# Kernel tuning notes

Hardware: AMD Instinct MI355X
Metric: run time of the kernel (lower is better)

Reference implementation:

```python
import jax, jax.numpy as jnp
import numpy as np
from jax import lax

STRIDES = (8, 16, 32, 64, 128)
LEVEL_HW = ((100, 128), (50, 64), (25, 32), (13, 16), (7, 8))
NUM_CLASSES = 80
PRE_NMS_THRESH = 0.05
PRE_NMS_TOPK = 1000
NMS_THRESH = 0.6
MAX_DET = 100
CLS_OFFSET = 1.0e4  # > max image coordinate, separates classes for joint NMS


def setup_inputs() -> dict:
    key = jax.random.key(0)
    B = 16
    ks = jax.random.split(key, 3 * len(LEVEL_HW))
    inp = {}
    i = 0
    for lvl, (h, w) in enumerate(LEVEL_HW):
        # shift logits down so sigmoid scores are mostly below the 0.05 candidate
        # threshold (realistic detection sparsity)
        inp[f"logits_p{lvl + 3}"] = jax.random.normal(ks[i], (B, NUM_CLASSES, h, w), jnp.float32) - 4.0; i += 1
        inp[f"bbox_p{lvl + 3}"] = jax.random.uniform(ks[i], (B, 4, h, w), jnp.float32, minval=0.0, maxval=64.0); i += 1
        inp[f"ctr_p{lvl + 3}"] = jax.random.normal(ks[i], (B, 1, h, w), jnp.float32); i += 1
    inp["im_info"] = jnp.tile(jnp.array([[800.0, 1024.0]], jnp.float32), (B, 1))
    return inp


def _locations(h, w, stride):
    # FCOSLocation: center of each stride cell -> [HW, 2] as (x, y)
    sx = jnp.arange(w, dtype=jnp.float32) * stride + stride // 2
    sy = jnp.arange(h, dtype=jnp.float32) * stride + stride // 2
    yy, xx = jnp.meshgrid(sy, sx, indexing="ij")
    return jnp.stack([xx.reshape(-1), yy.reshape(-1)], axis=-1)


def _nms_single(boxes, scores, classes):
    # boxes [K,4], scores [K] (descending), classes [K] int
    off = classes.astype(jnp.float32)[:, None] * CLS_OFFSET
    nb = boxes + off  # class-offset trick -> per-class NMS in one pass
    areas = jnp.maximum(nb[:, 2] - nb[:, 0], 0.0) * jnp.maximum(nb[:, 3] - nb[:, 1], 0.0)

    def body(sc, _):
        i = jnp.argmax(sc)
        s = sc[i]
        bi = nb[i]
        xx1 = jnp.maximum(bi[0], nb[:, 0])
        yy1 = jnp.maximum(bi[1], nb[:, 1])
        xx2 = jnp.minimum(bi[2], nb[:, 2])
        yy2 = jnp.minimum(bi[3], nb[:, 3])
        inter = jnp.maximum(xx2 - xx1, 0.0) * jnp.maximum(yy2 - yy1, 0.0)
        iou = inter / (areas[i] + areas - inter + 1e-9)
        sc2 = jnp.where(iou >= NMS_THRESH, -jnp.inf, sc).at[i].set(-jnp.inf)
        return sc2, (i, s > 0.0)

    _, (idxs, valid) = lax.scan(body, scores, None, length=MAX_DET)
    det = jnp.concatenate(
        [boxes[idxs], scores[idxs][:, None], classes[idxs].astype(jnp.float32)[:, None]],
        axis=-1,
    )  # [MAX_DET, 6] = x1,y1,x2,y2,score,class
    return jnp.where(valid[:, None], det, 0.0)


def _forward(logits_p3, bbox_p3, ctr_p3, logits_p4, bbox_p4, ctr_p4,
             logits_p5, bbox_p5, ctr_p5, logits_p6, bbox_p6, ctr_p6,
             logits_p7, bbox_p7, ctr_p7, im_info):
    levels = [(logits_p3, bbox_p3, ctr_p3), (logits_p4, bbox_p4, ctr_p4),
              (logits_p5, bbox_p5, ctr_p5), (logits_p6, bbox_p6, ctr_p6),
              (logits_p7, bbox_p7, ctr_p7)]
    scores_l, boxes_l = [], []
    for (lg, rg, ct), stride in zip(levels, STRIDES):
        B, C, H, W = lg.shape
        cls = jax.nn.sigmoid(lg).transpose(0, 2, 3, 1).reshape(B, H * W, C)
        cen = jax.nn.sigmoid(ct).transpose(0, 2, 3, 1).reshape(B, H * W, 1)
        # candidate threshold on raw class prob, then modulate by centerness
        comb = jnp.where(cls > PRE_NMS_THRESH, cls * cen, 0.0)
        locs = _locations(H, W, stride)  # [HW, 2]
        reg = rg.transpose(0, 2, 3, 1).reshape(B, H * W, 4)  # (l, t, r, b)
        bx = jnp.stack([locs[None, :, 0] - reg[..., 0],
                        locs[None, :, 1] - reg[..., 1],
                        locs[None, :, 0] + reg[..., 2],
                        locs[None, :, 1] + reg[..., 3]], axis=-1)
        scores_l.append(comb)
        boxes_l.append(bx)
    scores = jnp.concatenate(scores_l, axis=1)  # [B, N, C]
    boxes = jnp.concatenate(boxes_l, axis=1)    # [B, N, 4]
    B, N, C = scores.shape
    vals, idx = lax.top_k(scores.reshape(B, N * C), PRE_NMS_TOPK)  # [B, K]
    loc = idx // C
    cls_id = idx % C
    cand = jnp.take_along_axis(boxes, loc[..., None], axis=1)  # [B, K, 4]
    h = im_info[:, 0:1]
    w = im_info[:, 1:2]
    x1 = jnp.clip(cand[..., 0], 0.0, w - 1.0)
    y1 = jnp.clip(cand[..., 1], 0.0, h - 1.0)
    x2 = jnp.clip(cand[..., 2], 0.0, w - 1.0)
    y2 = jnp.clip(cand[..., 3], 0.0, h - 1.0)
    cand = jnp.stack([x1, y1, x2, y2], axis=-1)
    sc = jnp.where(vals > 0.0, jnp.sqrt(jnp.maximum(vals, 0.0) + 1e-12), 0.0)
    return jax.vmap(_nms_single)(cand, sc, cls_id)  # [B, MAX_DET, 6]


def reference(logits_p3, bbox_p3, ctr_p3, logits_p4, bbox_p4, ctr_p4,
              logits_p5, bbox_p5, ctr_p5, logits_p6, bbox_p6, ctr_p6,
              logits_p7, bbox_p7, ctr_p7, im_info):
    return _forward(logits_p3, bbox_p3, ctr_p3, logits_p4, bbox_p4, ctr_p4,
                    logits_p5, bbox_p5, ctr_p5, logits_p6, bbox_p6, ctr_p6,
                    logits_p7, bbox_p7, ctr_p7, im_info)
```

## Files before the change

### kernel.cpp

```cpp
#include <hip/hip_runtime.h>
#include <math.h>

#pragma clang fp contract(off)

#define NB 16
#define NC 80
#define NTOT 17064
#define TOPK 1000
#define NBINS 8192
#define CAP 4096
#define MAXDET 100
#define CNTSTRIDE 64
#define CHUNK 128
#define GH 128
#define SEGCAP 768
#define FB 16

struct Ptrs {
    const float* lg[5];
    const float* bb[5];
    const float* ct[5];
};

__device__ __forceinline__ void level_of(int n, int& l, int& hw, int& W,
                                         int& stride, int& half, int& HW) {
    if (n < 12800)      { l = 0; hw = n;         W = 128; stride = 8;   half = 4;  HW = 12800; }
    else if (n < 16000) { l = 1; hw = n - 12800; W = 64;  stride = 16;  half = 8;  HW = 3200;  }
    else if (n < 16800) { l = 2; hw = n - 16000; W = 32;  stride = 32;  half = 16; HW = 800;   }
    else if (n < 17008) { l = 3; hw = n - 16800; W = 16;  stride = 64;  half = 32; HW = 208;   }
    else                { l = 4; hw = n - 17008; W = 8;   stride = 128; half = 64; HW = 56;    }
}

__device__ __forceinline__ float fast_sig(float x) {
    float e = __expf(-x);
    return __builtin_amdgcn_rcpf(1.0f + e);
}

#define HG_ELEM(X, CT, J, CC, NB0)                                            \
    if ((X) > -2.47f) {                             \
        float cls = fast_sig(X);                                              \
        float cen = fast_sig(CT);                                             \
        unsigned bits = __float_as_uint(cls * cen);                           \
        if (bits >= FB_LO) {                                                  \
            int lb = (int)((bits - 32u) >> 19) - BINBASE;                     \
            lb = (lb < 0) ? 0 : ((lb > 63) ? 63 : lb);                        \
            atomicAdd(&whv[lb], 1u);                                          \
            unsigned pos = atomicAdd(s_na, 1u);                               \
            if (pos < SEGCAP) {                                               \
                unsigned idx = (unsigned)(((NB0) + (J)) * NC + (CC));         \
                segb[pos] = ((unsigned long long)bits << 32) | idx;           \
            }                                                                 \
        }                                                                     \
    }

template<int HW4, int NF4, int LVOFF>
__device__ __forceinline__ void histg_level(const float* lgb, const float* ctb,
        int tid, int bx, int gx, unsigned FB_LO, int BINBASE, unsigned* whv,
        unsigned* s_na, unsigned long long* segb) {
    for (int i0 = bx * 512; i0 < NF4; i0 += gx * 512) {
        int ia = i0 + tid, ib = i0 + 256 + tid;
        bool la = ia < NF4, lb2 = ib < NF4;
        float4 va = make_float4(-9.f, -9.f, -9.f, -9.f);
        float4 vb = make_float4(-9.f, -9.f, -9.f, -9.f);
        int hwa = 0, hwb = 0, cca = 0, ccb = 0;
        if (la) {
            cca = ia / HW4; hwa = ia - cca * HW4;
            va = *(const float4*)(lgb + cca * (HW4 * 4) + hwa * 4);
        }
        if (lb2) {
            ccb = ib / HW4; hwb = ib - ccb * HW4;
            vb = *(const float4*)(lgb + ccb * (HW4 * 4) + hwb * 4);
        }
        if (va.x > -2.47f || va.y > -2.47f || va.z > -2.47f || va.w > -2.47f) {
            float4 cv = *(const float4*)(ctb + hwa * 4);
            int nb0 = LVOFF + hwa * 4;
            HG_ELEM(va.x, cv.x, 0, cca, nb0) HG_ELEM(va.y, cv.y, 1, cca, nb0)
            HG_ELEM(va.z, cv.z, 2, cca, nb0) HG_ELEM(va.w, cv.w, 3, cca, nb0)
        }
        if (vb.x > -2.47f || vb.y > -2.47f || vb.z > -2.47f || vb.w > -2.47f) {
            float4 cv = *(const float4*)(ctb + hwb * 4);
            int nb0 = LVOFF + hwb * 4;
            HG_ELEM(vb.x, cv.x, 0, ccb, nb0) HG_ELEM(vb.y, cv.y, 1, ccb, nb0)
            HG_ELEM(vb.z, cv.z, 2, ccb, nb0) HG_ELEM(vb.w, cv.w, 3, ccb, nb0)
        }
    }
}
#undef HG_ELEM

__global__ void __launch_bounds__(256) k_histB(Ptrs p, unsigned* hist, unsigned* cnt2,
                                               unsigned* blkcnt, unsigned long long* segs) {
    __shared__ unsigned wh[4][64];
    __shared__ unsigned s_na;
    int b = blockIdx.y, tid = threadIdx.x, bx = blockIdx.x, gx = gridDim.x;
    int wv = tid >> 6;
    if (bx == 0 && tid == 0) cnt2[(size_t)b * CNTSTRIDE] = 0;
    ((unsigned*)wh)[tid] = 0;
    if (tid == 0) s_na = 0;
    __syncthreads();
    unsigned FB_LO = __float_as_uint(0.08f) - 64u;
    int BINBASE = (int)(__float_as_uint(0.08f) >> 19);
    unsigned* whv = wh[wv];
    unsigned long long* segb = segs + ((size_t)b * GH + bx) * SEGCAP;

    histg_level<3200, 256000,     0>(p.lg[0] + (size_t)b * NC * 12800, p.ct[0] + (size_t)b * 12800, tid, bx, gx, FB_LO, BINBASE, whv, &s_na, segb);
    histg_level< 800,  64000, 12800>(p.lg[1] + (size_t)b * NC * 3200,  p.ct[1] + (size_t)b * 3200,  tid, bx, gx, FB_LO, BINBASE, whv, &s_na, segb);
    histg_level< 200,  16000, 16000>(p.lg[2] + (size_t)b * NC * 800,   p.ct[2] + (size_t)b * 800,   tid, bx, gx, FB_LO, BINBASE, whv, &s_na, segb);
    histg_level<  52,   4160, 16800>(p.lg[3] + (size_t)b * NC * 208,   p.ct[3] + (size_t)b * 208,   tid, bx, gx, FB_LO, BINBASE, whv, &s_na, segb);
    histg_level<  14,   1120, 17008>(p.lg[4] + (size_t)b * NC * 56,    p.ct[4] + (size_t)b * 56,    tid, bx, gx, FB_LO, BINBASE, whv, &s_na, segb);

    __syncthreads();
    if (tid < 64) {
        unsigned s = wh[0][tid] + wh[1][tid] + wh[2][tid] + wh[3][tid];
        hist[((size_t)b * GH + bx) * 64 + tid] = s;
    }
    if (tid == 0) blkcnt[(size_t)b * GH + bx] = s_na;
}

template<int HW4, int NF4>
__device__ __forceinline__ void histf_level(const float* lgb, const float* ctb,
                                            int tid, unsigned* hist) {
    for (int i0 = 0; i0 < NF4; i0 += 256) {
        int i = i0 + tid;
        if (i < NF4) {
            int c = i / HW4, hwf = i - c * HW4;
            float4 v = *(const float4*)(lgb + c * (HW4 * 4) + hwf * 4);
            if (v.x > -2.95f || v.y > -2.95f || v.z > -2.95f || v.w > -2.95f) {
                float4 cv = *(const float4*)(ctb + hwf * 4);
                float xs[4] = {v.x, v.y, v.z, v.w};
                float cs[4] = {cv.x, cv.y, cv.z, cv.w};
#pragma unroll
                for (int j = 0; j < 4; ++j) {
                    float x = xs[j];
                    if (x > -2.95f) {
                        float cls = fast_sig(x);
                        if (cls > 0.04999f) {
                            bool in = true;
                            if (cls < 0.05001f)
                                in = (1.0f / (1.0f + expf(-x))) > 0.05f;
                            if (in) {
                                float cen = fast_sig(cs[j]);
                                unsigned bits = __float_as_uint(cls * cen);
                                unsigned cb = (bits > 32u) ? bits - 32u : 0u;
                                atomicAdd(&hist[cb >> 19], 1u);
                            }
                        }
                    }
                }
            }
        }
    }
}

#define CD_J(J, X, CT, NB0, CC, F, K)                                         \
    if ((X) > xpre) {                                                         \
        float cls = 1.0f / (1.0f + expf(-(X)));                               \
        if (cls > 0.05f) {                                                    \
            float cen = 1.0f / (1.0f + expf(-(CT)));                          \
            float comb = cls * cen;                                           \
            unsigned bits = __float_as_uint(comb);                            \
            if ((bits >> 19) >= Tb) {                                         \
                unsigned idx = (unsigned)(((NB0) + (J)) * NC + (CC));         \
                K = ((unsigned long long)bits << 32) | (0xFFFFFFFFu - idx);   \
                F = true;                                                     \
            }                                                                 \
        }                                                                     \
    }

template<int HW4, int NF4, int LVOFF>
__device__ __forceinline__ void compact_level(const float* lgb, const float* ctb,
        int tid, int lane, int bx, int gx, unsigned Tb, float xpre,
        unsigned* cntb, unsigned long long* selb, unsigned long long ltmask) {
    for (int i0 = bx * 512; i0 < NF4; i0 += gx * 512) {
        int ia = i0 + tid, ib2 = i0 + 256 + tid;
        bool la = ia < NF4, lb2 = ib2 < NF4;
        float4 va = make_float4(-9.f, -9.f, -9.f, -9.f);
        float4 vb = make_float4(-9.f, -9.f, -9.f, -9.f);
        int hwa = 0, hwb = 0, cca = 0, ccb = 0;
        if (la) {
            cca = ia / HW4; hwa = ia - cca * HW4;
            va = *(const float4*)(lgb + cca * (HW4 * 4) + hwa * 4);
        }
        if (lb2) {
            ccb = ib2 / HW4; hwb = ib2 - ccb * HW4;
            vb = *(const float4*)(lgb + ccb * (HW4 * 4) + hwb * 4);
        }
        {
            bool f0 = false, f1 = false, f2 = false, f3 = false;
            unsigned long long k0 = 0, k1 = 0, k2 = 0, k3 = 0;
            if (va.x > xpre || va.y > xpre || va.z > xpre || va.w > xpre) {
                float4 cv = *(const float4*)(ctb + hwa * 4);
                int nb0 = LVOFF + hwa * 4;
                CD_J(0, va.x, cv.x, nb0, cca, f0, k0)
                CD_J(1, va.y, cv.y, nb0, cca, f1, k1)
                CD_J(2, va.z, cv.z, nb0, cca, f2, k2)
                CD_J(3, va.w, cv.w, nb0, cca, f3, k3)
            }
            unsigned long long m0 = __ballot(f0), m1 = __ballot(f1);
            unsigned long long m2 = __ballot(f2), m3 = __ballot(f3);
            if (m0 | m1 | m2 | m3) {
                unsigned t0 = (unsigned)__popcll(m0), t1 = (unsigned)__popcll(m1);
                unsigned t2 = (unsigned)__popcll(m2), t3 = (unsigned)__popcll(m3);
                int basep = 0;
                if (lane == 0) basep = (int)atomicAdd(cntb, t0 + t1 + t2 + t3);
                basep = __shfl(basep, 0);
                if (f0) { int pos = basep + (int)__popcll(m0 & ltmask);                       if (pos < CAP) selb[pos] = k0; }
                if (f1) { int pos = basep + (int)t0 + (int)__popcll(m1 & ltmask);             if (pos < CAP) selb[pos] = k1; }
                if (f2) { int pos = basep + (int)(t0 + t1) + (int)__popcll(m2 & ltmask);      if (pos < CAP) selb[pos] = k2; }
                if (f3) { int pos = basep + (int)(t0 + t1 + t2) + (int)__popcll(m3 & ltmask); if (pos < CAP) selb[pos] = k3; }
            }
        }
        {
            bool f0 = false, f1 = false, f2 = false, f3 = false;
            unsigned long long k0 = 0, k1 = 0, k2 = 0, k3 = 0;
            if (vb.x > xpre || vb.y > xpre || vb.z > xpre || vb.w > xpre) {
                float4 cv = *(const float4*)(ctb + hwb * 4);
                int nb0 = LVOFF + hwb * 4;
                CD_J(0, vb.x, cv.x, nb0, ccb, f0, k0)
                CD_J(1, vb.y, cv.y, nb0, ccb, f1, k1)
                CD_J(2, vb.z, cv.z, nb0, ccb, f2, k2)
                CD_J(3, vb.w, cv.w, nb0, ccb, f3, k3)
            }
            unsigned long long m0 = __ballot(f0), m1 = __ballot(f1);
            unsigned long long m2 = __ballot(f2), m3 = __ballot(f3);
            if (m0 | m1 | m2 | m3) {
                unsigned t0 = (unsigned)__popcll(m0), t1 = (unsigned)__popcll(m1);
                unsigned t2 = (unsigned)__popcll(m2), t3 = (unsigned)__popcll(m3);
                int basep = 0;
                if (lane == 0) basep = (int)atomicAdd(cntb, t0 + t1 + t2 + t3);
                basep = __shfl(basep, 0);
                if (f0) { int pos = basep + (int)__popcll(m0 & ltmask);                       if (pos < CAP) selb[pos] = k0; }
                if (f1) { int pos = basep + (int)t0 + (int)__popcll(m1 & ltmask);             if (pos < CAP) selb[pos] = k1; }
                if (f2) { int pos = basep + (int)(t0 + t1) + (int)__popcll(m2 & ltmask);      if (pos < CAP) selb[pos] = k2; }
                if (f3) { int pos = basep + (int)(t0 + t1 + t2) + (int)__popcll(m3 & ltmask); if (pos < CAP) selb[pos] = k3; }
            }
        }
    }
}
#undef CD_J

__device__ __forceinline__ void run_compact(const Ptrs& p, int b, int tid, int lane,
        int bx, int gx, unsigned Tb, unsigned* cnt2, unsigned long long* sel) {
    float mthr = __uint_as_float(Tb << 19);
    float xpre = -2.95f;
    if (mthr > 1e-37f && mthr < 1.0f) {
        float lm = logf(mthr / (1.0f - mthr)) - 0.01f;
        if (lm > xpre) xpre = lm;
    }
    unsigned long long ltmask = (1ULL << lane) - 1ULL;
    unsigned* cntb = cnt2 + (size_t)b * CNTSTRIDE;
    unsigned long long* selb = sel + (size_t)b * CAP;
    compact_level<3200, 256000,     0>(p.lg[0] + (size_t)b * NC * 12800, p.ct[0] + (size_t)b * 12800, tid, lane, bx, gx, Tb, xpre, cntb, selb, ltmask);
    compact_level< 800,  64000, 12800>(p.lg[1] + (size_t)b * NC * 3200,  p.ct[1] + (size_t)b * 3200,  tid, lane, bx, gx, Tb, xpre, cntb, selb, ltmask);
    compact_level< 200,  16000, 16000>(p.lg[2] + (size_t)b * NC * 800,   p.ct[2] + (size_t)b * 800,   tid, lane, bx, gx, Tb, xpre, cntb, selb, ltmask);
    compact_level<  52,   4160, 16800>(p.lg[3] + (size_t)b * NC * 208,   p.ct[3] + (size_t)b * 208,   tid, lane, bx, gx, Tb, xpre, cntb, selb, ltmask);
    compact_level<  14,   1120, 17008>(p.lg[4] + (size_t)b * NC * 56,    p.ct[4] + (size_t)b * 56,    tid, lane, bx, gx, Tb, xpre, cntb, selb, ltmask);
}

__global__ void __launch_bounds__(256) k_filter(Ptrs p, const unsigned* hist,
        const unsigned* blkcnt, const unsigned long long* segs,
        unsigned* cnt2, unsigned long long* sel) {
    __shared__ unsigned part[4][64];
    __shared__ unsigned red[64];
    __shared__ unsigned fullh[NBINS];
    __shared__ int s_T, s_ok;
    __shared__ unsigned s_ovf;
    int b = blockIdx.y, tid = threadIdx.x, bx = blockIdx.x;
    int bin = tid & 63, grp = tid >> 6, lane = tid & 63;
    int BINBASE = (int)(__float_as_uint(0.08f) >> 19);

    unsigned s = 0;
    for (int blk = grp; blk < GH; blk += 4)
        s += hist[((size_t)b * GH + blk) * 64 + bin];
    part[grp][bin] = s;
    if (tid == 0) s_ovf = 0;
    __syncthreads();
    if (tid < 64) red[tid] = part[0][tid] + part[1][tid] + part[2][tid] + part[3][tid];
    unsigned ov = 0;
    for (int i = tid; i < GH; i += 256)
        ov |= (blkcnt[(size_t)b * GH + i] > SEGCAP) ? 1u : 0u;
    if (ov) atomicOr(&s_ovf, 1u);
    __syncthreads();
    if (tid == 0) {
        unsigned suf1 = 0;
        for (int i = 1; i < 64; ++i) suf1 += red[i];
        unsigned run = 0; int Tl = 0;
        for (int i = 63; i >= 1; --i) {
            run += red[i];
            if (run >= TOPK) { Tl = i; break; }
        }
        s_ok = (suf1 >= TOPK);
        s_T = Tl + BINBASE;
    }
    __syncthreads();

    if (s_ok && !s_ovf) {
        unsigned Tb = (unsigned)s_T;
        unsigned FLO = (Tb << 19) - 64u;
        unsigned* cntb = cnt2 + (size_t)b * CNTSTRIDE;
        unsigned long long* selb = sel + (size_t)b * CAP;
        unsigned long long ltmask = (1ULL << lane) - 1ULL;
        for (int sg = bx; sg < GH; sg += FB) {
            unsigned cs = blkcnt[(size_t)b * GH + sg];
            if (cs > SEGCAP) cs = SEGCAP;
            const unsigned long long* sp = segs + ((size_t)b * GH + sg) * SEGCAP;
            for (unsigned e0 = 0; e0 < cs; e0 += 256) {
                unsigned e = e0 + (unsigned)tid;
                bool take = false;
                unsigned long long key = 0;
                if (e < cs) {
                    unsigned long long kk = sp[e];
                    if ((unsigned)(kk >> 32) >= FLO) {
                        unsigned idx = (unsigned)kk;
                        int n = (int)(idx / NC), c = (int)(idx - (unsigned)n * NC);
                        int l, hw, W, stride, half, HW;
                        level_of(n, l, hw, W, stride, half, HW);
                        float x   = p.lg[l][(size_t)b * NC * HW + (size_t)c * HW + hw];
                        float ctv = p.ct[l][(size_t)b * HW + hw];
                        float cls = 1.0f / (1.0f + expf(-x));
                        if (cls > 0.05f) {
                            float cen = 1.0f / (1.0f + expf(-ctv));
                            unsigned bits = __float_as_uint(cls * cen);
                            if ((bits >> 19) >= Tb) {
                                key = ((unsigned long long)bits << 32) | (0xFFFFFFFFu - idx);
                                take = true;
                            }
                        }
                    }
                }
                unsigned long long m = __ballot(take);
                if (m) {
                    unsigned tot = (unsigned)__popcll(m);
                    int basep = 0;
                    if (lane == 0) basep = (int)atomicAdd(cntb, tot);
                    basep = __shfl(basep, 0);
                    if (take) {
                        int pos = basep + (int)__popcll(m & ltmask);
                        if (pos < CAP) selb[pos] = key;
                    }
                }
            }
        }
        return;
    }

    if (!s_ok) {
        if (bx != 0) return;
        for (int i = tid; i < NBINS; i += 256) fullh[i] = 0;
        __syncthreads();
        histf_level<3200, 256000>(p.lg[0] + (size_t)b * NC * 12800, p.ct[0] + (size_t)b * 12800, tid, fullh);
        histf_level< 800,  64000>(p.lg[1] + (size_t)b * NC * 3200,  p.ct[1] + (size_t)b * 3200,  tid, fullh);
        histf_level< 200,  16000>(p.lg[2] + (size_t)b * NC * 800,   p.ct[2] + (size_t)b * 800,   tid, fullh);
        histf_level<  52,   4160>(p.lg[3] + (size_t)b * NC * 208,   p.ct[3] + (size_t)b * 208,   tid, fullh);
        histf_level<  14,   1120>(p.lg[4] + (size_t)b * NC * 56,    p.ct[4] + (size_t)b * 56,    tid, fullh);
        __syncthreads();
        if (tid == 0) {
            unsigned run = 0; int Tf = 0;
            for (int i = NBINS - 1; i >= 0; --i) {
                run += fullh[i];
                if (run >= TOPK) { Tf = i; break; }
            }
            s_T = Tf;
        }
        __syncthreads();
        run_compact(p, b, tid, lane, 0, 1, (unsigned)s_T, cnt2, sel);
        return;
    }

    run_compact(p, b, tid, lane, bx, FB, (unsigned)s_T, cnt2, sel);
}

__global__ void __launch_bounds__(256) k_rankdec(Ptrs p, const unsigned* cnt,
                                                 const unsigned long long* sel,
                                                 const float* im_info, float* cand) {
    __shared__ __align__(16) unsigned long long keys[CAP];
    int b = blockIdx.y, tid = threadIdx.x;
    unsigned M = cnt[(size_t)b * CNTSTRIDE];
    if (M > CAP) M = CAP;
    int s0 = blockIdx.x * 256;
    if (s0 >= (int)M) return;
    int Mpad = (int)((M + 1u) & ~1u);
    for (int i = tid; i < Mpad; i += 256)
        keys[i] = (i < (int)M) ? sel[(size_t)b * CAP + i] : 0ULL;
    __syncthreads();

    int s = s0 + tid;
    if (s >= (int)M) return;
    unsigned long long k = keys[s];
    int rank = 0;
    for (int j = 0; j < Mpad; j += 2) {
        ulonglong2 kk = *(const ulonglong2*)&keys[j];
        rank += (kk.x > k) ? 1 : 0;
        rank += (kk.y > k) ? 1 : 0;
    }
    if (rank >= TOPK) return;

    float Him = im_info[b * 2 + 0], Wim = im_info[b * 2 + 1];
    float xmax = Wim - 1.0f, ymax = Him - 1.0f;
    unsigned sb = (unsigned)(k >> 32);
    unsigned idx = 0xFFFFFFFFu - (unsigned)(k & 0xFFFFFFFFu);
    float val = __uint_as_float(sb);
    int n = idx / NC, c = idx - n * NC;
    int l, hw, W, stride, half, HW;
    level_of(n, l, hw, W, stride, half, HW);
    int wx = hw % W, hy = hw / W;
    float locx = (float)(wx * stride + half);
    float locy = (float)(hy * stride + half);
    const float* bb = p.bb[l] + (size_t)b * 4 * HW + hw;
    float r0 = bb[0], r1 = bb[(size_t)HW], r2 = bb[(size_t)2 * HW], r3 = bb[(size_t)3 * HW];
    float x1 = locx - r0, y1 = locy - r1, x2 = locx + r2, y2 = locy + r3;
    x1 = fminf(fmaxf(x1, 0.f), xmax);
    y1 = fminf(fmaxf(y1, 0.f), ymax);
    x2 = fminf(fmaxf(x2, 0.f), xmax);
    y2 = fminf(fmaxf(y2, 0.f), ymax);
    float scv = sqrtf(val + 1e-12f);
    float off = (float)c * 10000.0f;
    float a0 = x1 + off, a1 = y1 + off, a2 = x2 + off, a3 = y2 + off;
    float area = fmaxf(a2 - a0, 0.f) * fmaxf(a3 - a1, 0.f);
    float* dst = cand + ((size_t)b * TOPK + rank) * 12;
    *(float4*)(dst + 0) = make_float4(x1, y1, x2, y2);
    *(float4*)(dst + 4) = make_float4(a0, a1, a2, a3);
    *(float4*)(dst + 8) = make_float4(area, scv, (float)c, 0.f);
}

__global__ void __launch_bounds__(64) k_nms(const unsigned* cnt, const float* cand,
                                            float* out) {
    __shared__ float4 s_ob[CHUNK], s_nb[CHUNK], s_ms[CHUNK];
    int b = blockIdx.x, lane = threadIdx.x;
    unsigned M = cnt[(size_t)b * CNTSTRIDE];
    if (M > CAP) M = CAP;
    int ncand = (int)M < TOPK ? (int)M : TOPK;
    const float* src = cand + (size_t)b * TOPK * 12;
    float* ob = out + (size_t)b * MAXDET * 6;

    int na = 0;
    float4 a0b = make_float4(0.f, 0.f, 0.f, 0.f);
    float4 a1b = make_float4(0.f, 0.f, 0.f, 0.f);
    float a0a = 0.f, a1a = 0.f;

    for (int base = 0; base < ncand && na < MAXDET; base += CHUNK) {
        int cn = ncand - base; if (cn > CHUNK) cn = CHUNK;
        for (int cidx = lane; cidx < cn; cidx += 64) {
            const float* s = src + (size_t)(base + cidx) * 12;
            s_ob[cidx] = *(const float4*)(s + 0);
            s_nb[cidx] = *(const float4*)(s + 4);
            s_ms[cidx] = *(const float4*)(s + 8);
        }
        __syncthreads();
        for (int r = 0; r < cn && na < MAXDET; ++r) {
            float4 cb = s_nb[r];
            float ca = s_ms[r].x;
            bool sup = false;
            if (lane < na) {
                float xx1 = fmaxf(a0b.x, cb.x);
                float yy1 = fmaxf(a0b.y, cb.y);
                float xx2 = fminf(a0b.z, cb.z);
                float yy2 = fminf(a0b.w, cb.w);
                float inter = fmaxf(xx2 - xx1, 0.f) * fmaxf(yy2 - yy1, 0.f);
                float iou = inter / (((a0a + ca) - inter) + 1e-9f);
                sup = (iou >= 0.6f);
            }
            if (lane + 64 < na) {
                float xx1 = fmaxf(a1b.x, cb.x);
                float yy1 = fmaxf(a1b.y, cb.y);
                float xx2 = fminf(a1b.z, cb.z);
                float yy2 = fminf(a1b.w, cb.w);
                float inter = fmaxf(xx2 - xx1, 0.f) * fmaxf(yy2 - yy1, 0.f);
                float iou = inter / (((a1a + ca) - inter) + 1e-9f);
                sup |= (iou >= 0.6f);
            }
            if (__ballot(sup) == 0ULL) {
                if (lane == (na & 63)) {
                    if (na < 64) { a0b = cb; a0a = ca; }
                    else         { a1b = cb; a1a = ca; }
                }
                if (lane == 0) {
                    float4 o4 = s_ob[r]; float4 m4 = s_ms[r];
                    ob[na * 6 + 0] = o4.x; ob[na * 6 + 1] = o4.y;
                    ob[na * 6 + 2] = o4.z; ob[na * 6 + 3] = o4.w;
                    ob[na * 6 + 4] = m4.y; ob[na * 6 + 5] = m4.z;
                }
                ++na;
            }
        }
        __syncthreads();
    }
    for (int q = na * 6 + lane; q < MAXDET * 6; q += 64)
        ob[q] = 0.f;
}

extern "C" void kernel_launch(void* const* d_in, const int* in_sizes, int n_in,
                              void* d_out, int out_size, void* d_ws, size_t ws_size,
                              hipStream_t stream) {
    Ptrs p;
    for (int l = 0; l < 5; ++l) {
        p.lg[l] = (const float*)d_in[3 * l + 0];
        p.bb[l] = (const float*)d_in[3 * l + 1];
        p.ct[l] = (const float*)d_in[3 * l + 2];
    }
    const float* im_info = (const float*)d_in[15];
    float* out = (float*)d_out;
    unsigned char* w = (unsigned char*)d_ws;

    unsigned* hist          = (unsigned*)(w);
    unsigned* cnt2          = (unsigned*)(w + 524288);
    unsigned* blkcnt        = (unsigned*)(w + 528384);
    unsigned long long* segs = (unsigned long long*)(w + 536576);
    unsigned long long* sel = (unsigned long long*)(w + 13119488);
    float* cand             = (float*)(w + 13643776);

    k_histB<<<dim3(GH, NB), 256, 0, stream>>>(p, hist, cnt2, blkcnt, segs);
    k_filter<<<dim3(FB, NB), 256, 0, stream>>>(p, hist, blkcnt, segs, cnt2, sel);
    k_rankdec<<<dim3(16, NB), 256, 0, stream>>>(p, cnt2, sel, im_info, cand);
    k_nms<<<NB, 64, 0, stream>>>(cnt2, cand, out);
}
```

Before: 241.4 us.

## Replace block-shared atomic segment counter with per-wave ballot compaction

The histogram kernel now gives each wavefront its own candidate segment and computes write positions with ballot and popcount, replacing the per-element shared-memory atomic on a block counter. Sigmoid scores are computed branch-free for all eight elements, and the centerness vector is loaded unconditionally. The filter kernel is changed to walk per-wave segments with one wave per segment. This removes contended LDS atomics but adds unconditional sigmoid math and centerness loads. It also uses a larger workspace layout with smaller per-wave caps, so a wave that overflows its cap is more likely.

New measurement: 227.1 us. 5.9% less time.

```diff
diff --git a/kernel.cpp b/kernel.cpp
--- a/kernel.cpp
+++ b/kernel.cpp
@@ -13,7 +13,7 @@
 #define CNTSTRIDE 64
 #define CHUNK 128
 #define GH 128
-#define SEGCAP 768
+#define WSEGCAP 256
 #define FB 16
 
 struct Ptrs {
@@ -36,84 +36,102 @@
     return __builtin_amdgcn_rcpf(1.0f + e);
 }
 
-#define HG_ELEM(X, CT, J, CC, NB0)                                            \
-    if ((X) > -2.47f) {                             \
-        float cls = fast_sig(X);                                              \
-        float cen = fast_sig(CT);                                             \
-        unsigned bits = __float_as_uint(cls * cen);                           \
-        if (bits >= FB_LO) {                                                  \
-            int lb = (int)((bits - 32u) >> 19) - BINBASE;                     \
-            lb = (lb < 0) ? 0 : ((lb > 63) ? 63 : lb);                        \
-            atomicAdd(&whv[lb], 1u);                                          \
-            unsigned pos = atomicAdd(s_na, 1u);                               \
-            if (pos < SEGCAP) {                                               \
-                unsigned idx = (unsigned)(((NB0) + (J)) * NC + (CC));         \
-                segb[pos] = ((unsigned long long)bits << 32) | idx;           \
-            }                                                                 \
+#define HG_EMIT(BITS, NN, CC, POS)                                            \
+    {                                                                         \
+        int lb = (int)(((BITS) - 32u) >> 19) - BINBASE;                       \
+        lb = (lb < 0) ? 0 : ((lb > 63) ? 63 : lb);                            \
+        atomicAdd(&whv[lb], 1u);             \
+        unsigned pos_ = (POS);                                                \
+        if (pos_ < WSEGCAP) {                                                 \
+            unsigned idx_ = (unsigned)((NN) * NC + (CC));                     \
+            segw[pos_] = ((unsigned long long)(BITS) << 32) | idx_;           \
         }                                                                     \
     }
 
 template<int HW4, int NF4, int LVOFF>
 __device__ __forceinline__ void histg_level(const float* lgb, const float* ctb,
         int tid, int bx, int gx, unsigned FB_LO, int BINBASE, unsigned* whv,
-        unsigned* s_na, unsigned long long* segb) {
+        unsigned& wcnt, unsigned long long* segw, unsigned long long ltmask) {
     for (int i0 = bx * 512; i0 < NF4; i0 += gx * 512) {
         int ia = i0 + tid, ib = i0 + 256 + tid;
         bool la = ia < NF4, lb2 = ib < NF4;
-        float4 va = make_float4(-9.f, -9.f, -9.f, -9.f);
-        float4 vb = make_float4(-9.f, -9.f, -9.f, -9.f);
+        float4 va = make_float4(-40.f, -40.f, -40.f, -40.f);
+        float4 vb = make_float4(-40.f, -40.f, -40.f, -40.f);
+        float4 ca = make_float4(0.f, 0.f, 0.f, 0.f);
+        float4 cb = make_float4(0.f, 0.f, 0.f, 0.f);
         int hwa = 0, hwb = 0, cca = 0, ccb = 0;
         if (la) {
             cca = ia / HW4; hwa = ia - cca * HW4;
             va = *(const float4*)(lgb + cca * (HW4 * 4) + hwa * 4);
+            ca = *(const float4*)(ctb + hwa * 4);
         }
         if (lb2) {
             ccb = ib / HW4; hwb = ib - ccb * HW4;
             vb = *(const float4*)(lgb + ccb * (HW4 * 4) + hwb * 4);
-        }
-        if (va.x > -2.47f || va.y > -2.47f || va.z > -2.47f || va.w > -2.47f) {
-            float4 cv = *(const float4*)(ctb + hwa * 4);
-            int nb0 = LVOFF + hwa * 4;
-            HG_ELEM(va.x, cv.x, 0, cca, nb0) HG_ELEM(va.y, cv.y, 1, cca, nb0)
-            HG_ELEM(va.z, cv.z, 2, cca, nb0) HG_ELEM(va.w, cv.w, 3, cca, nb0)
-        }
-        if (vb.x > -2.47f || vb.y > -2.47f || vb.z > -2.47f || vb.w > -2.47f) {
-            float4 cv = *(const float4*)(ctb + hwb * 4);
-            int nb0 = LVOFF + hwb * 4;
-            HG_ELEM(vb.x, cv.x, 0, ccb, nb0) HG_ELEM(vb.y, cv.y, 1, ccb, nb0)
-            HG_ELEM(vb.z, cv.z, 2, ccb, nb0) HG_ELEM(vb.w, cv.w, 3, ccb, nb0)
-        }
-    }
-}
-#undef HG_ELEM
+            cb = *(const float4*)(ctb + hwb * 4);
+        }
+        unsigned b0 = __float_as_uint(fast_sig(va.x) * fast_sig(ca.x));
+        unsigned b1 = __float_as_uint(fast_sig(va.y) * fast_sig(ca.y));
+        unsigned b2 = __float_as_uint(fast_sig(va.z) * fast_sig(ca.z));
+        unsigned b3 = __float_as_uint(fast_sig(va.w) * fast_sig(ca.w));
+        unsigned b4 = __float_as_uint(fast_sig(vb.x) * fast_sig(cb.x));
+        unsigned b5 = __float_as_uint(fast_sig(vb.y) * fast_sig(cb.y));
+        unsigned b6 = __float_as_uint(fast_sig(vb.z) * fast_sig(cb.z));
+        unsigned b7 = __float_as_uint(fast_sig(vb.w) * fast_sig(cb.w));
+        bool f0 = b0 >= FB_LO, f1 = b1 >= FB_LO, f2 = b2 >= FB_LO, f3 = b3 >= FB_LO;
+        bool f4 = b4 >= FB_LO, f5 = b5 >= FB_LO, f6 = b6 >= FB_LO, f7 = b7 >= FB_LO;
+        unsigned long long m0 = __ballot(f0), m1 = __ballot(f1);
+        unsigned long long m2 = __ballot(f2), m3 = __ballot(f3);
+        unsigned long long m4 = __ballot(f4), m5 = __ballot(f5);
+        unsigned long long m6 = __ballot(f6), m7 = __ballot(f7);
+        if (m0 | m1 | m2 | m3 | m4 | m5 | m6 | m7) {
+            unsigned t0 = (unsigned)__popcll(m0), t1 = (unsigned)__popcll(m1);
+            unsigned t2 = (unsigned)__popcll(m2), t3 = (unsigned)__popcll(m3);
+            unsigned t4 = (unsigned)__popcll(m4), t5 = (unsigned)__popcll(m5);
+            unsigned t6 = (unsigned)__popcll(m6), t7 = (unsigned)__popcll(m7);
+            unsigned wb = wcnt;
+            wcnt = wb + t0 + t1 + t2 + t3 + t4 + t5 + t6 + t7;
+            int nb0a = LVOFF + hwa * 4, nb0b = LVOFF + hwb * 4;
+            if (f0) HG_EMIT(b0, nb0a + 0, cca, wb + (unsigned)__popcll(m0 & ltmask))
+            if (f1) HG_EMIT(b1, nb0a + 1, cca, wb + t0 + (unsigned)__popcll(m1 & ltmask))
+            if (f2) HG_EMIT(b2, nb0a + 2, cca, wb + t0 + t1 + (unsigned)__popcll(m2 & ltmask))
+            if (f3) HG_EMIT(b3, nb0a + 3, cca, wb + t0 + t1 + t2 + (unsigned)__popcll(m3 & ltmask))
+            if (f4) HG_EMIT(b4, nb0b + 0, ccb, wb + t0 + t1 + t2 + t3 + (unsigned)__popcll(m4 & ltmask))
+            if (f5) HG_EMIT(b5, nb0b + 1, ccb, wb + t0 + t1 + t2 + t3 + t4 + (unsigned)__popcll(m5 & ltmask))
+            if (f6) HG_EMIT(b6, nb0b + 2, ccb, wb + t0 + t1 + t2 + t3 + t4 + t5 + (unsigned)__popcll(m6 & ltmask))
+            if (f7) HG_EMIT(b7, nb0b + 3, ccb, wb + t0 + t1 + t2 + t3 + t4 + t5 + t6 + (unsigned)__popcll(m7 & ltmask))
+        }
+    }
+}
+#undef HG_EMIT
 
 __global__ void __launch_bounds__(256) k_histB(Ptrs p, unsigned* hist, unsigned* cnt2,
-                                               unsigned* blkcnt, unsigned long long* segs) {
+                                               unsigned* wavecnt, unsigned long long* segs) {
     __shared__ unsigned wh[4][64];
-    __shared__ unsigned s_na;
     int b = blockIdx.y, tid = threadIdx.x, bx = blockIdx.x, gx = gridDim.x;
-    int wv = tid >> 6;
+    int wv = tid >> 6, lane = tid & 63;
     if (bx == 0 && tid == 0) cnt2[(size_t)b * CNTSTRIDE] = 0;
     ((unsigned*)wh)[tid] = 0;
-    if (tid == 0) s_na = 0;
-    __syncthreads();
     unsigned FB_LO = __float_as_uint(0.08f) - 64u;
     int BINBASE = (int)(__float_as_uint(0.08f) >> 19);
     unsigned* whv = wh[wv];
-    unsigned long long* segb = segs + ((size_t)b * GH + bx) * SEGCAP;
-
-    histg_level<3200, 256000,     0>(p.lg[0] + (size_t)b * NC * 12800, p.ct[0] + (size_t)b * 12800, tid, bx, gx, FB_LO, BINBASE, whv, &s_na, segb);
-    histg_level< 800,  64000, 12800>(p.lg[1] + (size_t)b * NC * 3200,  p.ct[1] + (size_t)b * 3200,  tid, bx, gx, FB_LO, BINBASE, whv, &s_na, segb);
-    histg_level< 200,  16000, 16000>(p.lg[2] + (size_t)b * NC * 800,   p.ct[2] + (size_t)b * 800,   tid, bx, gx, FB_LO, BINBASE, whv, &s_na, segb);
-    histg_level<  52,   4160, 16800>(p.lg[3] + (size_t)b * NC * 208,   p.ct[3] + (size_t)b * 208,   tid, bx, gx, FB_LO, BINBASE, whv, &s_na, segb);
-    histg_level<  14,   1120, 17008>(p.lg[4] + (size_t)b * NC * 56,    p.ct[4] + (size_t)b * 56,    tid, bx, gx, FB_LO, BINBASE, whv, &s_na, segb);
-
+    unsigned long long ltmask = (1ULL << lane) - 1ULL;
+    unsigned wcnt = 0;
+    unsigned long long* segw = segs + (((size_t)b * GH + bx) * 4 + wv) * WSEGCAP;
+
+    histg_level<3200, 256000,     0>(p.lg[0] + (size_t)b * NC * 12800, p.ct[0] + (size_t)b * 12800, tid, bx, gx, FB_LO, BINBASE, whv, wcnt, segw, ltmask);
+    histg_level< 800,  64000, 12800>(p.lg[1] + (size_t)b * NC * 3200,  p.ct[1] + (size_t)b * 3200,  tid, bx, gx, FB_LO, BINBASE, whv, wcnt, segw, ltmask);
+    histg_level< 200,  16000, 16000>(p.lg[2] + (size_t)b * NC * 800,   p.ct[2] + (size_t)b * 800,   tid, bx, gx, FB_LO, BINBASE, whv, wcnt, segw, ltmask);
+    histg_level<  52,   4160, 16800>(p.lg[3] + (size_t)b * NC * 208,   p.ct[3] + (size_t)b * 208,   tid, bx, gx, FB_LO, BINBASE, whv, wcnt, segw, ltmask);
+    histg_level<  14,   1120, 17008>(p.lg[4] + (size_t)b * NC * 56,    p.ct[4] + (size_t)b * 56,    tid, bx, gx, FB_LO, BINBASE, whv, wcnt, segw, ltmask);
+
+    if (lane == 0)
+        wavecnt[((size_t)b * GH + bx) * 4 + wv] = wcnt;
     __syncthreads();
     if (tid < 64) {
         unsigned s = wh[0][tid] + wh[1][tid] + wh[2][tid] + wh[3][tid];
         hist[((size_t)b * GH + bx) * 64 + tid] = s;
     }
-    if (tid == 0) blkcnt[(size_t)b * GH + bx] = s_na;
 }
 
 template<int HW4, int NF4>
@@ -257,7 +275,7 @@
 }
 
 __global__ void __launch_bounds__(256) k_filter(Ptrs p, const unsigned* hist,
-        const unsigned* blkcnt, const unsigned long long* segs,
+        const unsigned* wavecnt, const unsigned long long* segs,
         unsigned* cnt2, unsigned long long* sel) {
     __shared__ unsigned part[4][64];
     __shared__ unsigned red[64];
@@ -265,7 +283,7 @@
     __shared__ int s_T, s_ok;
     __shared__ unsigned s_ovf;
     int b = blockIdx.y, tid = threadIdx.x, bx = blockIdx.x;
-    int bin = tid & 63, grp = tid >> 6, lane = tid & 63;
+    int bin = tid & 63, grp = tid >> 6, lane = tid & 63, wv = tid >> 6;
     int BINBASE = (int)(__float_as_uint(0.08f) >> 19);
 
     unsigned s = 0;
@@ -276,8 +294,8 @@
     __syncthreads();
     if (tid < 64) red[tid] = part[0][tid] + part[1][tid] + part[2][tid] + part[3][tid];
     unsigned ov = 0;
-    for (int i = tid; i < GH; i += 256)
-        ov |= (blkcnt[(size_t)b * GH + i] > SEGCAP) ? 1u : 0u;
+    for (int i = tid; i < GH * 4; i += 256)
+        ov |= (wavecnt[(size_t)b * GH * 4 + i] > WSEGCAP) ? 1u : 0u;
     if (ov) atomicOr(&s_ovf, 1u);
     __syncthreads();
     if (tid == 0) {
@@ -299,12 +317,12 @@
         unsigned* cntb = cnt2 + (size_t)b * CNTSTRIDE;
         unsigned long long* selb = sel + (size_t)b * CAP;
         unsigned long long ltmask = (1ULL << lane) - 1ULL;
-        for (int sg = bx; sg < GH; sg += FB) {
-            unsigned cs = blkcnt[(size_t)b * GH + sg];
-            if (cs > SEGCAP) cs = SEGCAP;
-            const unsigned long long* sp = segs + ((size_t)b * GH + sg) * SEGCAP;
-            for (unsigned e0 = 0; e0 < cs; e0 += 256) {
-                unsigned e = e0 + (unsigned)tid;
+        for (int sg = bx * 4 + wv; sg < GH * 4; sg += FB * 4) {
+            unsigned cs = wavecnt[(size_t)b * GH * 4 + sg];
+            if (cs > WSEGCAP) cs = WSEGCAP;
+            const unsigned long long* sp = segs + ((size_t)b * GH * 4 + sg) * WSEGCAP;
+            for (unsigned e0 = 0; e0 < cs; e0 += 64) {
+                unsigned e = e0 + (unsigned)lane;
                 bool take = false;
                 unsigned long long key = 0;
                 if (e < cs) {
@@ -501,15 +519,15 @@
     float* out = (float*)d_out;
     unsigned char* w = (unsigned char*)d_ws;
 
-    unsigned* hist          = (unsigned*)(w);
-    unsigned* cnt2          = (unsigned*)(w + 524288);
-    unsigned* blkcnt        = (unsigned*)(w + 528384);
-    unsigned long long* segs = (unsigned long long*)(w + 536576);
-    unsigned long long* sel = (unsigned long long*)(w + 13119488);
-    float* cand             = (float*)(w + 13643776);
-
-    k_histB<<<dim3(GH, NB), 256, 0, stream>>>(p, hist, cnt2, blkcnt, segs);
-    k_filter<<<dim3(FB, NB), 256, 0, stream>>>(p, hist, blkcnt, segs, cnt2, sel);
+    unsigned* hist           = (unsigned*)(w);
+    unsigned* cnt2           = (unsigned*)(w + 524288);
+    unsigned* wavecnt        = (unsigned*)(w + 528384);
+    unsigned long long* segs = (unsigned long long*)(w + 561152);
+    unsigned long long* sel  = (unsigned long long*)(w + 17338368);
+    float* cand              = (float*)(w + 17862656);
+
+    k_histB<<<dim3(GH, NB), 256, 0, stream>>>(p, hist, cnt2, wavecnt, segs);
+    k_filter<<<dim3(FB, NB), 256, 0, stream>>>(p, hist, wavecnt, segs, cnt2, sel);
     k_rankdec<<<dim3(16, NB), 256, 0, stream>>>(p, cnt2, sel, im_info, cand);
     k_nms<<<NB, 64, 0, stream>>>(cnt2, cand, out);
 }
```
